# Performance work log

Measured on AMD Instinct MI355X. Metric: run time of the kernel, lower is better.

The kernel has to match this reference:

```python
import jax, jax.numpy as jnp
import numpy as np

B, T, D = 1, 1024, 2048
F_DIM = 1408
E = 8
TOPK = 2


def setup_inputs() -> dict:
    key = jax.random.key(0)
    ks = jax.random.split(key, 5)
    x = jax.random.normal(ks[0], (B, T, D), dtype=jnp.float32)
    # torch nn.Linear weight layout: [out_features, in_features]
    gate_w = jax.random.normal(ks[1], (E, D), dtype=jnp.float32) * 0.02
    gate_proj = jax.random.normal(ks[2], (E, F_DIM, D), dtype=jnp.float32) * 0.02
    up_proj = jax.random.normal(ks[3], (E, F_DIM, D), dtype=jnp.float32) * 0.02
    down_proj = jax.random.normal(ks[4], (E, D, F_DIM), dtype=jnp.float32) * 0.02
    return {"x": x, "gate_w": gate_w, "gate_proj": gate_proj,
            "up_proj": up_proj, "down_proj": down_proj}


def reference(x, gate_w, gate_proj, up_proj, down_proj):
    b, t, d = x.shape
    x_flat = x.reshape(-1, d)                                  # [N, D]
    n = x_flat.shape[0]
    # Router: top-k logits then softmax over the selected k.
    router_logits = x_flat @ gate_w.T                          # [N, E]
    top_w, sel = jax.lax.top_k(router_logits, TOPK)            # [N, K]
    top_w = jax.nn.softmax(top_w, axis=-1)                     # [N, K]
    # Scatter routing weights into dense per-token expert weights [N, E].
    tok_ids = jnp.arange(n)[:, None]
    tw = jnp.zeros((n, E), dtype=x.dtype).at[tok_ids, sel].add(top_w)
    # Dense expert compute (mathematically identical: unselected experts get
    # zero combine weight). SwiGLU per expert.
    g = jnp.einsum('nd,efd->enf', x_flat, gate_proj)           # [E, N, F]
    u = jnp.einsum('nd,efd->enf', x_flat, up_proj)             # [E, N, F]
    h = jax.nn.silu(g) * u                                     # [E, N, F]
    eo = jnp.einsum('enf,edf->end', h, down_proj)              # [E, N, D]
    out = jnp.einsum('end,ne->nd', eo, tw)                     # [N, D]
    return out.reshape(b, t, d)
```

## Files before the change

### kernel.cpp

```cpp
#include <hip/hip_runtime.h>
#include <hip/hip_bf16.h>
#include <stdint.h>

typedef __attribute__((ext_vector_type(8))) short short8;
typedef __attribute__((ext_vector_type(4))) float f32x4;
typedef unsigned int u32;
typedef unsigned short u16;

static constexpr int N_TOK = 1024;
static constexpr int DDIM = 2048;
static constexpr int FDIM = 1408;
static constexpr int NEXP = 8;
static constexpr int MAXROWS = 3072;
static constexpr int NT128 = 24;

static constexpr size_t O_META   = 0;
static constexpr size_t O_TE128  = 256;
static constexpr size_t O_TR128  = 384;
static constexpr size_t O_ROWTOK = 768;
static constexpr size_t O_TOKROWS= O_ROWTOK + (size_t)MAXROWS * 4;
static constexpr size_t O_SEL    = O_TOKROWS + 2048 * 4;
static constexpr size_t O_W      = O_SEL + 2048 * 4;
static constexpr size_t O_H      = (O_W + 2048 * 4 + 255) & ~(size_t)255;
static constexpr size_t O_EO     = O_H + (size_t)MAXROWS * FDIM * 2;

static __device__ __forceinline__ u16 f2bf(float f) {
    return __builtin_bit_cast(u16, __float2bfloat16(f));
}
static __device__ __forceinline__ float bf2f(u16 s) {
    u32 u = ((u32)s) << 16;
    return __builtin_bit_cast(float, u);
}
static __device__ __forceinline__ u32 pack2(float a, float b) {
    return (u32)f2bf(a) | ((u32)f2bf(b) << 16);
}

__global__ __launch_bounds__(256) void router_kernel(
    const float* __restrict__ x, const float* __restrict__ gw,
    int* __restrict__ sel, float* __restrict__ wout)
{
    __shared__ float xs[DDIM];
    __shared__ float lg[NEXP];
    const int tok = blockIdx.x;
    const float* xr = x + (size_t)tok * DDIM;
    for (int i = threadIdx.x; i < DDIM / 4; i += 256)
        ((float4*)xs)[i] = ((const float4*)xr)[i];
    __syncthreads();
    const int wid = threadIdx.x >> 6, lane = threadIdx.x & 63;
    for (int i = 0; i < 2; i++) {
        const int e = wid * 2 + i;
        const float* g = gw + (size_t)e * DDIM;
        float s = 0.f;
        for (int k = lane; k < DDIM; k += 64) s += xs[k] * g[k];
        for (int off = 32; off > 0; off >>= 1) s += __shfl_down(s, off);
        if (lane == 0) lg[e] = s;
    }
    __syncthreads();
    if (threadIdx.x == 0) {
        int i1 = 0;
        for (int e = 1; e < NEXP; e++) if (lg[e] > lg[i1]) i1 = e;
        int i2 = -1;
        for (int e = 0; e < NEXP; e++) {
            if (e == i1) continue;
            if (i2 < 0 || lg[e] > lg[i2]) i2 = e;
        }
        const float e2 = __expf(lg[i2] - lg[i1]);
        const float w1 = 1.f / (1.f + e2);
        sel[tok * 2] = i1; sel[tok * 2 + 1] = i2;
        wout[tok * 2] = w1; wout[tok * 2 + 1] = e2 * w1;
    }
}

__global__ __launch_bounds__(512) void build_kernel(
    const int* __restrict__ sel,
    int* __restrict__ meta, int* __restrict__ te128, int* __restrict__ tr128,
    int* __restrict__ row_tok, int* __restrict__ tok_rows)
{
    __shared__ int s0[N_TOK], s1[N_TOK];
    __shared__ u16 p0[N_TOK], p1[N_TOK];
    __shared__ int counts[NEXP], offs[NEXP];
    for (int i = threadIdx.x; i < N_TOK; i += 512) {
        s0[i] = sel[i * 2]; s1[i] = sel[i * 2 + 1];
    }
    __syncthreads();
    const int e = threadIdx.x >> 6, lane = threadIdx.x & 63;
    int base = 0;
    for (int c = 0; c < N_TOK / 64; c++) {
        const int tk = c * 64 + lane;
        const int slot = (s0[tk] == e) ? 0 : ((s1[tk] == e) ? 1 : -1);
        const unsigned long long m = __ballot(slot >= 0);
        const int pre = __popcll(m & ((1ull << lane) - 1ull));
        if (slot == 0) p0[tk] = (u16)(base + pre);
        else if (slot == 1) p1[tk] = (u16)(base + pre);
        base += __popcll(m);
    }
    if (lane == 0) counts[e] = base;
    __syncthreads();
    if (threadIdx.x == 0) {
        int off = 0, n128 = 0;
        for (int qq = 0; qq < NEXP; qq++) {
            offs[qq] = off;
            const int pc = (counts[qq] + 127) & ~127;
            for (int i = 0; i < pc / 128; i++) { te128[n128] = qq; tr128[n128] = off + i * 128; n128++; }
            off += pc;
        }
        meta[0] = n128; meta[1] = off;
    }
    __syncthreads();
    const int off = offs[e];
    for (int c = 0; c < N_TOK / 64; c++) {
        const int tk = c * 64 + lane;
        const int slot = (s0[tk] == e) ? 0 : ((s1[tk] == e) ? 1 : -1);
        if (slot >= 0) {
            const int row = off + (slot ? p1[tk] : p0[tk]);
            row_tok[row] = tk;
            tok_rows[tk * 2 + slot] = row;
        }
    }
    const int cnt = counts[e];
    const int pc = (cnt + 127) & ~127;
    for (int p = cnt + lane; p < pc; p += 64) row_tok[off + p] = -1;
}

__global__ __launch_bounds__(512, 4) void mlp1_kernel(
    const float* __restrict__ x,
    const float* __restrict__ gp, const float* __restrict__ upw,
    u16* __restrict__ h,
    const int* __restrict__ meta, const int* __restrict__ te128,
    const int* __restrict__ tr128, const int* __restrict__ row_tok)
{
    const int tile = blockIdx.y;
    const int nb = blockIdx.x;
    if (tile >= meta[0]) return;
    const int n0 = nb * 64;
    const int e = te128[tile];
    const int r0g = tr128[tile];

    __shared__ __align__(16) u16 As[2][128 * 64];
    __shared__ __align__(16) u16 Bs0[2][64 * 64];
    __shared__ __align__(16) u16 Bs1[2][64 * 64];

    const int t = threadIdx.x;
    const int r16 = t >> 4, c4 = t & 15;

    const float* arow[4]; bool avalid[4];
    #pragma unroll
    for (int i = 0; i < 4; i++) {
        const int tok = row_tok[r0g + r16 + 32 * i];
        avalid[i] = (tok >= 0);
        arow[i] = x + (size_t)(tok < 0 ? 0 : tok) * DDIM + c4 * 4;
    }
    const float* brow0[2];
    const float* brow1[2];
    {
        const float* B0 = gp + (size_t)e * FDIM * DDIM;
        const float* B1 = upw + (size_t)e * FDIM * DDIM;
        #pragma unroll
        for (int i = 0; i < 2; i++) {
            brow0[i] = B0 + (size_t)(n0 + r16 + 32 * i) * DDIM + c4 * 4;
            brow1[i] = B1 + (size_t)(n0 + r16 + 32 * i) * DDIM + c4 * 4;
        }
    }
    int sOffA[4], sOffB[2];
    #pragma unroll
    for (int i = 0; i < 4; i++) {
        const int row = r16 + 32 * i;
        sOffA[i] = row * 64 + (((c4 >> 1) ^ (row & 7)) * 8) + (c4 & 1) * 4;
    }
    #pragma unroll
    for (int i = 0; i < 2; i++) {
        const int row = r16 + 32 * i;
        sOffB[i] = row * 64 + (((c4 >> 1) ^ (row & 7)) * 8) + (c4 & 1) * 4;
    }

    const int wid = t >> 6, lane = t & 63;
    const int wm = (wid >> 1) * 32, wn = (wid & 1) * 32;
    const int lr = lane & 15, lhi = lane >> 4;

    f32x4 acc0[2][2], acc1[2][2];
    #pragma unroll
    for (int m = 0; m < 2; m++)
        #pragma unroll
        for (int n = 0; n < 2; n++) {
            acc0[m][n] = f32x4{0.f, 0.f, 0.f, 0.f};
            acc1[m][n] = f32x4{0.f, 0.f, 0.f, 0.f};
        }

    float4 pa[4], pb0[2], pb1[2];

    auto LOAD = [&](int k0) {
        #pragma unroll
        for (int i = 0; i < 4; i++)
            pa[i] = avalid[i] ? *(const float4*)(arow[i] + k0)
                              : make_float4(0.f, 0.f, 0.f, 0.f);
        #pragma unroll
        for (int i = 0; i < 2; i++) pb0[i] = *(const float4*)(brow0[i] + k0);
        #pragma unroll
        for (int i = 0; i < 2; i++) pb1[i] = *(const float4*)(brow1[i] + k0);
    };
    auto STORE = [&](int bsel) {
        #pragma unroll
        for (int i = 0; i < 4; i++) {
            uint2 v; v.x = pack2(pa[i].x, pa[i].y); v.y = pack2(pa[i].z, pa[i].w);
            *(uint2*)(&As[bsel][sOffA[i]]) = v;
        }
        #pragma unroll
        for (int i = 0; i < 2; i++) {
            uint2 v; v.x = pack2(pb0[i].x, pb0[i].y); v.y = pack2(pb0[i].z, pb0[i].w);
            *(uint2*)(&Bs0[bsel][sOffB[i]]) = v;
        }
        #pragma unroll
        for (int i = 0; i < 2; i++) {
            uint2 v; v.x = pack2(pb1[i].x, pb1[i].y); v.y = pack2(pb1[i].z, pb1[i].w);
            *(uint2*)(&Bs1[bsel][sOffB[i]]) = v;
        }
    };
    auto COMPUTE = [&](int bsel) {
        #pragma unroll
        for (int ks = 0; ks < 2; ks++) {
            short8 a[2], b0[2], b1[2];
            #pragma unroll
            for (int m = 0; m < 2; m++) {
                const int row = wm + m * 16 + lr;
                const int gr = (ks * 4 + lhi) ^ (row & 7);
                a[m] = *(const short8*)(&As[bsel][row * 64 + gr * 8]);
            }
            #pragma unroll
            for (int n = 0; n < 2; n++) {
                const int row = wn + n * 16 + lr;
                const int gr = (ks * 4 + lhi) ^ (row & 7);
                b0[n] = *(const short8*)(&Bs0[bsel][row * 64 + gr * 8]);
                b1[n] = *(const short8*)(&Bs1[bsel][row * 64 + gr * 8]);
            }
            #pragma unroll
            for (int m = 0; m < 2; m++)
                #pragma unroll
                for (int n = 0; n < 2; n++) {
                    acc0[m][n] = __builtin_amdgcn_mfma_f32_16x16x32_bf16(a[m], b0[n], acc0[m][n], 0, 0, 0);
                    acc1[m][n] = __builtin_amdgcn_mfma_f32_16x16x32_bf16(a[m], b1[n], acc1[m][n], 0, 0, 0);
                }
        }
    };

    constexpr int NT = DDIM / 64;
    LOAD(0); STORE(0);
    __syncthreads();
    for (int kt = 0; kt < NT; kt++) {
        const int cur = kt & 1;
        if (kt + 1 < NT) LOAD((kt + 1) * 64);
        COMPUTE(cur);
        if (kt + 1 < NT) {
            STORE(cur ^ 1);
            __syncthreads();
        }
    }

    #pragma unroll
    for (int m = 0; m < 2; m++) {
        const int rowb = r0g + wm + m * 16 + lhi * 4;
        #pragma unroll
        for (int n = 0; n < 2; n++) {
            const int col = n0 + wn + n * 16 + lr;
            #pragma unroll
            for (int j = 0; j < 4; j++) {
                const float g = acc0[m][n][j], u = acc1[m][n][j];
                const float hv = g / (1.f + __expf(-g)) * u;
                h[(size_t)(rowb + j) * FDIM + col] = f2bf(hv);
            }
        }
    }
}

__global__ __launch_bounds__(512, 4) void down_kernel(
    const u16* __restrict__ h, const float* __restrict__ dp,
    u16* __restrict__ eo,
    const int* __restrict__ meta, const int* __restrict__ te128,
    const int* __restrict__ tr128)
{
    const int tile = blockIdx.y;
    const int nb = blockIdx.x;
    if (tile >= meta[0]) return;
    const int n0 = nb * 128;
    const int e = te128[tile];
    const int r0g = tr128[tile];

    __shared__ __align__(16) u16 As[2][128 * 64];
    __shared__ __align__(16) u16 Bs[2][128 * 64];

    const int t = threadIdx.x;
    const int r8 = t >> 3, g8 = t & 7;
    const int r16 = t >> 4, c4 = t & 15;

    const u16* arow[2];
    int sOffA[2];
    #pragma unroll
    for (int i = 0; i < 2; i++) {
        const int row = r8 + 64 * i;
        arow[i] = h + (size_t)(r0g + row) * FDIM + g8 * 8;
        sOffA[i] = row * 64 + ((g8 ^ (row & 7)) * 8);
    }
    const float* brow[4];
    int sOffB[4];
    {
        const float* B = dp + (size_t)e * DDIM * FDIM;
        #pragma unroll
        for (int i = 0; i < 4; i++) {
            const int row = r16 + 32 * i;
            brow[i] = B + (size_t)(n0 + row) * FDIM + c4 * 4;
            sOffB[i] = row * 64 + (((c4 >> 1) ^ (row & 7)) * 8) + (c4 & 1) * 4;
        }
    }

    const int wid = t >> 6, lane = t & 63;
    const int wm = (wid >> 2) * 64, wn = (wid & 3) * 32;
    const int lr = lane & 15, lhi = lane >> 4;

    f32x4 acc[4][2];
    #pragma unroll
    for (int m = 0; m < 4; m++)
        #pragma unroll
        for (int n = 0; n < 2; n++)
            acc[m][n] = f32x4{0.f, 0.f, 0.f, 0.f};

    uint4 pa[2]; float4 pb[4];

    auto LOAD = [&](int k0) {
        #pragma unroll
        for (int i = 0; i < 2; i++) pa[i] = *(const uint4*)(arow[i] + k0);
        #pragma unroll
        for (int i = 0; i < 4; i++) pb[i] = *(const float4*)(brow[i] + k0);
    };
    auto STORE = [&](int bsel) {
        #pragma unroll
        for (int i = 0; i < 2; i++) *(uint4*)(&As[bsel][sOffA[i]]) = pa[i];
        #pragma unroll
        for (int i = 0; i < 4; i++) {
            uint2 v; v.x = pack2(pb[i].x, pb[i].y); v.y = pack2(pb[i].z, pb[i].w);
            *(uint2*)(&Bs[bsel][sOffB[i]]) = v;
        }
    };
    auto COMPUTE = [&](int bsel) {
        #pragma unroll
        for (int ks = 0; ks < 2; ks++) {
            short8 a[4], b[2];
            #pragma unroll
            for (int m = 0; m < 4; m++) {
                const int row = wm + m * 16 + lr;
                const int gr = (ks * 4 + lhi) ^ (row & 7);
                a[m] = *(const short8*)(&As[bsel][row * 64 + gr * 8]);
            }
            #pragma unroll
            for (int n = 0; n < 2; n++) {
                const int row = wn + n * 16 + lr;
                const int gr = (ks * 4 + lhi) ^ (row & 7);
                b[n] = *(const short8*)(&Bs[bsel][row * 64 + gr * 8]);
            }
            #pragma unroll
            for (int m = 0; m < 4; m++)
                #pragma unroll
                for (int n = 0; n < 2; n++)
                    acc[m][n] = __builtin_amdgcn_mfma_f32_16x16x32_bf16(a[m], b[n], acc[m][n], 0, 0, 0);
        }
    };

    constexpr int NT = FDIM / 64;
    LOAD(0); STORE(0);
    __syncthreads();
    for (int kt = 0; kt < NT; kt++) {
        const int cur = kt & 1;
        if (kt + 1 < NT) LOAD((kt + 1) * 64);
        COMPUTE(cur);
        if (kt + 1 < NT) {
            STORE(cur ^ 1);
            __syncthreads();
        }
    }

    #pragma unroll
    for (int m = 0; m < 4; m++) {
        const int rowb = r0g + wm + m * 16 + lhi * 4;
        #pragma unroll
        for (int n = 0; n < 2; n++) {
            const int col = n0 + wn + n * 16 + lr;
            #pragma unroll
            for (int j = 0; j < 4; j++)
                eo[(size_t)(rowb + j) * DDIM + col] = f2bf(acc[m][n][j]);
        }
    }
}

__global__ __launch_bounds__(256) void combine_kernel(
    const u16* __restrict__ eo, const int* __restrict__ tok_rows,
    const float* __restrict__ w, float* __restrict__ out)
{
    const int tok = blockIdx.x;
    const int r1 = tok_rows[tok * 2], r2 = tok_rows[tok * 2 + 1];
    const float w1 = w[tok * 2], w2 = w[tok * 2 + 1];
    const int d = threadIdx.x * 8;
    const uint4 a = *(const uint4*)(eo + (size_t)r1 * DDIM + d);
    const uint4 b = *(const uint4*)(eo + (size_t)r2 * DDIM + d);
    const u32 av[4] = {a.x, a.y, a.z, a.w};
    const u32 bv[4] = {b.x, b.y, b.z, b.w};
    float4 o0, o1;
    float* op[8] = {&o0.x, &o0.y, &o0.z, &o0.w, &o1.x, &o1.y, &o1.z, &o1.w};
    #pragma unroll
    for (int i = 0; i < 4; i++) {
        *op[2 * i]     = w1 * bf2f((u16)(av[i] & 0xffff)) + w2 * bf2f((u16)(bv[i] & 0xffff));
        *op[2 * i + 1] = w1 * bf2f((u16)(av[i] >> 16))    + w2 * bf2f((u16)(bv[i] >> 16));
    }
    float4* po = (float4*)(out + (size_t)tok * DDIM + d);
    po[0] = o0; po[1] = o1;
}

extern "C" void kernel_launch(void* const* d_in, const int* in_sizes, int n_in,
                              void* d_out, int out_size, void* d_ws, size_t ws_size,
                              hipStream_t stream) {
    const float* x  = (const float*)d_in[0];
    const float* gw = (const float*)d_in[1];
    const float* gp = (const float*)d_in[2];
    const float* up = (const float*)d_in[3];
    const float* dp = (const float*)d_in[4];
    float* out = (float*)d_out;
    char* ws = (char*)d_ws;

    int*   meta     = (int*)(ws + O_META);
    int*   te128    = (int*)(ws + O_TE128);
    int*   tr128    = (int*)(ws + O_TR128);
    int*   row_tok  = (int*)(ws + O_ROWTOK);
    int*   tok_rows = (int*)(ws + O_TOKROWS);
    int*   sel      = (int*)(ws + O_SEL);
    float* w        = (float*)(ws + O_W);
    u16*   h        = (u16*)(ws + O_H);
    u16*   eo       = (u16*)(ws + O_EO);

    router_kernel<<<N_TOK, 256, 0, stream>>>(x, gw, sel, w);
    build_kernel<<<1, 512, 0, stream>>>(sel, meta, te128, tr128, row_tok, tok_rows);
    mlp1_kernel<<<dim3(FDIM / 64, NT128), 512, 0, stream>>>(
        x, gp, up, h, meta, te128, tr128, row_tok);
    down_kernel<<<dim3(DDIM / 128, NT128), 512, 0, stream>>>(
        h, dp, eo, meta, te128, tr128);
    combine_kernel<<<N_TOK, 256, 0, stream>>>(eo, tok_rows, w, out);
}
```

Baseline: 196.8 us.

## Stage fp32 weights via direct global-to-LDS loads and shrink GEMM tiles

Both expert GEMM kernels now copy fp32 weight tiles straight into shared memory with global_load_lds, and convert them to bf16 when reading fragments instead of before the shared-memory store. Output tiles drop from 64/128 columns to 32 with a K step of 32, so far more blocks launch and each wave handles a single 16-row slice. The aim is to cut register staging and VALU conversion work on the load path and to raise parallelism. In exchange, each block reuses its activation tile less, activations are re-read more often, the K loop has twice as many iterations and barriers, and the per-fragment conversion is repeated.

```diff
diff --git a/kernel.cpp b/kernel.cpp
--- a/kernel.cpp
+++ b/kernel.cpp
@@ -33,6 +33,11 @@
 }
 static __device__ __forceinline__ u32 pack2(float a, float b) {
     return (u32)f2bf(a) | ((u32)f2bf(b) << 16);
+}
+static __device__ __forceinline__ void gload16(const void* g, void* l) {
+    __builtin_amdgcn_global_load_lds(
+        (const __attribute__((address_space(1))) void*)g,
+        (__attribute__((address_space(3))) void*)l, 16, 0, 0);
 }
 
 __global__ __launch_bounds__(256) void router_kernel(
@@ -122,7 +127,7 @@
     for (int p = cnt + lane; p < pc; p += 64) row_tok[off + p] = -1;
 }
 
-__global__ __launch_bounds__(512, 4) void mlp1_kernel(
+__global__ __launch_bounds__(512) void mlp1_kernel(
     const float* __restrict__ x,
     const float* __restrict__ gp, const float* __restrict__ upw,
     u16* __restrict__ h,
@@ -132,146 +137,98 @@
     const int tile = blockIdx.y;
     const int nb = blockIdx.x;
     if (tile >= meta[0]) return;
-    const int n0 = nb * 64;
+    const int n0 = nb * 32;
     const int e = te128[tile];
     const int r0g = tr128[tile];
 
-    __shared__ __align__(16) u16 As[2][128 * 64];
-    __shared__ __align__(16) u16 Bs0[2][64 * 64];
-    __shared__ __align__(16) u16 Bs1[2][64 * 64];
+    __shared__ __align__(16) u16 As[2][128 * 40];
+    __shared__ __align__(16) float Bs[2][2][32 * 32];
 
     const int t = threadIdx.x;
-    const int r16 = t >> 4, c4 = t & 15;
-
-    const float* arow[4]; bool avalid[4];
-    #pragma unroll
-    for (int i = 0; i < 4; i++) {
-        const int tok = row_tok[r0g + r16 + 32 * i];
-        avalid[i] = (tok >= 0);
-        arow[i] = x + (size_t)(tok < 0 ? 0 : tok) * DDIM + c4 * 4;
-    }
-    const float* brow0[2];
-    const float* brow1[2];
-    {
-        const float* B0 = gp + (size_t)e * FDIM * DDIM;
-        const float* B1 = upw + (size_t)e * FDIM * DDIM;
-        #pragma unroll
-        for (int i = 0; i < 2; i++) {
-            brow0[i] = B0 + (size_t)(n0 + r16 + 32 * i) * DDIM + c4 * 4;
-            brow1[i] = B1 + (size_t)(n0 + r16 + 32 * i) * DDIM + c4 * 4;
-        }
-    }
-    int sOffA[4], sOffB[2];
-    #pragma unroll
-    for (int i = 0; i < 4; i++) {
-        const int row = r16 + 32 * i;
-        sOffA[i] = row * 64 + (((c4 >> 1) ^ (row & 7)) * 8) + (c4 & 1) * 4;
-    }
-    #pragma unroll
-    for (int i = 0; i < 2; i++) {
-        const int row = r16 + 32 * i;
-        sOffB[i] = row * 64 + (((c4 >> 1) ^ (row & 7)) * 8) + (c4 & 1) * 4;
-    }
-
     const int wid = t >> 6, lane = t & 63;
-    const int wm = (wid >> 1) * 32, wn = (wid & 1) * 32;
     const int lr = lane & 15, lhi = lane >> 4;
 
-    f32x4 acc0[2][2], acc1[2][2];
-    #pragma unroll
-    for (int m = 0; m < 2; m++)
+    const int ar = t >> 2, ag = t & 3;
+    const int tokA = row_tok[r0g + ar];
+    const bool av = (tokA >= 0);
+    const float* asrc = x + (size_t)(av ? tokA : 0) * DDIM + ag * 8;
+    const int aoff = ar * 40 + ag * 8;
+
+    const int bmat = wid >> 2, wloc = wid & 3;
+    const int brow = wloc * 8 + (lane >> 3);
+    const int bgs = (lane & 7) ^ (brow & 7);
+    const float* bsrc = (bmat ? upw : gp) + (size_t)e * FDIM * DDIM
+                      + (size_t)(n0 + brow) * DDIM + bgs * 4;
+
+    f32x4 acc0[2], acc1[2];
+    acc0[0] = acc0[1] = acc1[0] = acc1[1] = f32x4{0.f, 0.f, 0.f, 0.f};
+    float4 pa0, pa1;
+
+    auto LOADA = [&](int k0) {
+        pa0 = av ? *(const float4*)(asrc + k0)     : make_float4(0.f, 0.f, 0.f, 0.f);
+        pa1 = av ? *(const float4*)(asrc + k0 + 4) : make_float4(0.f, 0.f, 0.f, 0.f);
+    };
+    auto STOREA = [&](int bsel) {
+        uint4 v;
+        v.x = pack2(pa0.x, pa0.y); v.y = pack2(pa0.z, pa0.w);
+        v.z = pack2(pa1.x, pa1.y); v.w = pack2(pa1.z, pa1.w);
+        *(uint4*)(&As[bsel][aoff]) = v;
+    };
+    auto STAGEB = [&](int bsel, int k0) {
+        gload16(bsrc + k0, &Bs[bmat][bsel][wloc * 256]);
+    };
+    auto COMPUTE = [&](int bsel) {
+        const int rowa = wid * 16 + lr;
+        const short8 a = *(const short8*)(&As[bsel][rowa * 40 + lhi * 8]);
         #pragma unroll
         for (int n = 0; n < 2; n++) {
-            acc0[m][n] = f32x4{0.f, 0.f, 0.f, 0.f};
-            acc1[m][n] = f32x4{0.f, 0.f, 0.f, 0.f};
-        }
-
-    float4 pa[4], pb0[2], pb1[2];
-
-    auto LOAD = [&](int k0) {
-        #pragma unroll
-        for (int i = 0; i < 4; i++)
-            pa[i] = avalid[i] ? *(const float4*)(arow[i] + k0)
-                              : make_float4(0.f, 0.f, 0.f, 0.f);
-        #pragma unroll
-        for (int i = 0; i < 2; i++) pb0[i] = *(const float4*)(brow0[i] + k0);
-        #pragma unroll
-        for (int i = 0; i < 2; i++) pb1[i] = *(const float4*)(brow1[i] + k0);
-    };
-    auto STORE = [&](int bsel) {
-        #pragma unroll
-        for (int i = 0; i < 4; i++) {
-            uint2 v; v.x = pack2(pa[i].x, pa[i].y); v.y = pack2(pa[i].z, pa[i].w);
-            *(uint2*)(&As[bsel][sOffA[i]]) = v;
-        }
-        #pragma unroll
-        for (int i = 0; i < 2; i++) {
-            uint2 v; v.x = pack2(pb0[i].x, pb0[i].y); v.y = pack2(pb0[i].z, pb0[i].w);
-            *(uint2*)(&Bs0[bsel][sOffB[i]]) = v;
-        }
-        #pragma unroll
-        for (int i = 0; i < 2; i++) {
-            uint2 v; v.x = pack2(pb1[i].x, pb1[i].y); v.y = pack2(pb1[i].z, pb1[i].w);
-            *(uint2*)(&Bs1[bsel][sOffB[i]]) = v;
-        }
-    };
-    auto COMPUTE = [&](int bsel) {
-        #pragma unroll
-        for (int ks = 0; ks < 2; ks++) {
-            short8 a[2], b0[2], b1[2];
+            const int rb = n * 16 + lr;
+            const int g0 = ((lhi << 1)    ) ^ (rb & 7);
+            const int g1 = ((lhi << 1) | 1) ^ (rb & 7);
             #pragma unroll
-            for (int m = 0; m < 2; m++) {
-                const int row = wm + m * 16 + lr;
-                const int gr = (ks * 4 + lhi) ^ (row & 7);
-                a[m] = *(const short8*)(&As[bsel][row * 64 + gr * 8]);
+            for (int mat = 0; mat < 2; mat++) {
+                const f32x4 lo = *(const f32x4*)(&Bs[mat][bsel][rb * 32 + g0 * 4]);
+                const f32x4 hi = *(const f32x4*)(&Bs[mat][bsel][rb * 32 + g1 * 4]);
+                uint4 q;
+                q.x = pack2(lo[0], lo[1]); q.y = pack2(lo[2], lo[3]);
+                q.z = pack2(hi[0], hi[1]); q.w = pack2(hi[2], hi[3]);
+                const short8 b = __builtin_bit_cast(short8, q);
+                if (mat == 0)
+                    acc0[n] = __builtin_amdgcn_mfma_f32_16x16x32_bf16(a, b, acc0[n], 0, 0, 0);
+                else
+                    acc1[n] = __builtin_amdgcn_mfma_f32_16x16x32_bf16(a, b, acc1[n], 0, 0, 0);
             }
-            #pragma unroll
-            for (int n = 0; n < 2; n++) {
-                const int row = wn + n * 16 + lr;
-                const int gr = (ks * 4 + lhi) ^ (row & 7);
-                b0[n] = *(const short8*)(&Bs0[bsel][row * 64 + gr * 8]);
-                b1[n] = *(const short8*)(&Bs1[bsel][row * 64 + gr * 8]);
-            }
-            #pragma unroll
-            for (int m = 0; m < 2; m++)
-                #pragma unroll
-                for (int n = 0; n < 2; n++) {
-                    acc0[m][n] = __builtin_amdgcn_mfma_f32_16x16x32_bf16(a[m], b0[n], acc0[m][n], 0, 0, 0);
-                    acc1[m][n] = __builtin_amdgcn_mfma_f32_16x16x32_bf16(a[m], b1[n], acc1[m][n], 0, 0, 0);
-                }
-        }
-    };
-
-    constexpr int NT = DDIM / 64;
-    LOAD(0); STORE(0);
+        }
+    };
+
+    constexpr int NT = DDIM / 32;
+    STAGEB(0, 0); LOADA(0); STOREA(0);
     __syncthreads();
     for (int kt = 0; kt < NT; kt++) {
         const int cur = kt & 1;
-        if (kt + 1 < NT) LOAD((kt + 1) * 64);
+        const bool more = (kt + 1 < NT);
+        if (more) { LOADA((kt + 1) * 32); STAGEB(cur ^ 1, (kt + 1) * 32); }
         COMPUTE(cur);
-        if (kt + 1 < NT) {
-            STORE(cur ^ 1);
+        if (more) {
+            STOREA(cur ^ 1);
             __syncthreads();
         }
     }
 
     #pragma unroll
-    for (int m = 0; m < 2; m++) {
-        const int rowb = r0g + wm + m * 16 + lhi * 4;
+    for (int n = 0; n < 2; n++) {
+        const int col = n0 + n * 16 + lr;
         #pragma unroll
-        for (int n = 0; n < 2; n++) {
-            const int col = n0 + wn + n * 16 + lr;
-            #pragma unroll
-            for (int j = 0; j < 4; j++) {
-                const float g = acc0[m][n][j], u = acc1[m][n][j];
-                const float hv = g / (1.f + __expf(-g)) * u;
-                h[(size_t)(rowb + j) * FDIM + col] = f2bf(hv);
-            }
-        }
-    }
-}
-
-__global__ __launch_bounds__(512, 4) void down_kernel(
+        for (int j = 0; j < 4; j++) {
+            const int row = r0g + wid * 16 + lhi * 4 + j;
+            const float g = acc0[n][j], u = acc1[n][j];
+            const float hv = g / (1.f + __expf(-g)) * u;
+            h[(size_t)row * FDIM + col] = f2bf(hv);
+        }
+    }
+}
+
+__global__ __launch_bounds__(512) void down_kernel(
     const u16* __restrict__ h, const float* __restrict__ dp,
     u16* __restrict__ eo,
     const int* __restrict__ meta, const int* __restrict__ te128,
@@ -280,111 +237,74 @@
     const int tile = blockIdx.y;
     const int nb = blockIdx.x;
     if (tile >= meta[0]) return;
-    const int n0 = nb * 128;
+    const int n0 = nb * 32;
     const int e = te128[tile];
     const int r0g = tr128[tile];
 
-    __shared__ __align__(16) u16 As[2][128 * 64];
-    __shared__ __align__(16) u16 Bs[2][128 * 64];
+    __shared__ __align__(16) u16 As[2][128 * 40];
+    __shared__ __align__(16) float Bs[2][32 * 32];
 
     const int t = threadIdx.x;
-    const int r8 = t >> 3, g8 = t & 7;
-    const int r16 = t >> 4, c4 = t & 15;
-
-    const u16* arow[2];
-    int sOffA[2];
-    #pragma unroll
-    for (int i = 0; i < 2; i++) {
-        const int row = r8 + 64 * i;
-        arow[i] = h + (size_t)(r0g + row) * FDIM + g8 * 8;
-        sOffA[i] = row * 64 + ((g8 ^ (row & 7)) * 8);
-    }
-    const float* brow[4];
-    int sOffB[4];
-    {
-        const float* B = dp + (size_t)e * DDIM * FDIM;
+    const int wid = t >> 6, lane = t & 63;
+    const int lr = lane & 15, lhi = lane >> 4;
+
+    const int ar = t >> 2, ag = t & 3;
+    const u16* asrc = h + (size_t)(r0g + ar) * FDIM + ag * 8;
+    const int aoff = ar * 40 + ag * 8;
+
+    const int brow = (wid & 3) * 8 + (lane >> 3);
+    const int bgs = (lane & 7) ^ (brow & 7);
+    const float* bsrc = dp + (size_t)e * DDIM * FDIM
+                      + (size_t)(n0 + brow) * FDIM + bgs * 4;
+
+    f32x4 acc[2];
+    acc[0] = acc[1] = f32x4{0.f, 0.f, 0.f, 0.f};
+    uint4 pa;
+
+    auto LOADA = [&](int k0u) { pa = *(const uint4*)(asrc + k0u); };
+    auto STOREA = [&](int bsel) { *(uint4*)(&As[bsel][aoff]) = pa; };
+    auto STAGEB = [&](int bsel, int k0) {
+        if (wid < 4) gload16(bsrc + k0, &Bs[bsel][(wid & 3) * 256]);
+    };
+    auto COMPUTE = [&](int bsel) {
+        const int rowa = wid * 16 + lr;
+        const short8 a = *(const short8*)(&As[bsel][rowa * 40 + lhi * 8]);
         #pragma unroll
-        for (int i = 0; i < 4; i++) {
-            const int row = r16 + 32 * i;
-            brow[i] = B + (size_t)(n0 + row) * FDIM + c4 * 4;
-            sOffB[i] = row * 64 + (((c4 >> 1) ^ (row & 7)) * 8) + (c4 & 1) * 4;
-        }
-    }
-
-    const int wid = t >> 6, lane = t & 63;
-    const int wm = (wid >> 2) * 64, wn = (wid & 3) * 32;
-    const int lr = lane & 15, lhi = lane >> 4;
-
-    f32x4 acc[4][2];
-    #pragma unroll
-    for (int m = 0; m < 4; m++)
-        #pragma unroll
-        for (int n = 0; n < 2; n++)
-            acc[m][n] = f32x4{0.f, 0.f, 0.f, 0.f};
-
-    uint4 pa[2]; float4 pb[4];
-
-    auto LOAD = [&](int k0) {
-        #pragma unroll
-        for (int i = 0; i < 2; i++) pa[i] = *(const uint4*)(arow[i] + k0);
-        #pragma unroll
-        for (int i = 0; i < 4; i++) pb[i] = *(const float4*)(brow[i] + k0);
-    };
-    auto STORE = [&](int bsel) {
-        #pragma unroll
-        for (int i = 0; i < 2; i++) *(uint4*)(&As[bsel][sOffA[i]]) = pa[i];
-        #pragma unroll
-        for (int i = 0; i < 4; i++) {
-            uint2 v; v.x = pack2(pb[i].x, pb[i].y); v.y = pack2(pb[i].z, pb[i].w);
-            *(uint2*)(&Bs[bsel][sOffB[i]]) = v;
-        }
-    };
-    auto COMPUTE = [&](int bsel) {
-        #pragma unroll
-        for (int ks = 0; ks < 2; ks++) {
-            short8 a[4], b[2];
-            #pragma unroll
-            for (int m = 0; m < 4; m++) {
-                const int row = wm + m * 16 + lr;
-                const int gr = (ks * 4 + lhi) ^ (row & 7);
-                a[m] = *(const short8*)(&As[bsel][row * 64 + gr * 8]);
-            }
-            #pragma unroll
-            for (int n = 0; n < 2; n++) {
-                const int row = wn + n * 16 + lr;
-                const int gr = (ks * 4 + lhi) ^ (row & 7);
-                b[n] = *(const short8*)(&Bs[bsel][row * 64 + gr * 8]);
-            }
-            #pragma unroll
-            for (int m = 0; m < 4; m++)
-                #pragma unroll
-                for (int n = 0; n < 2; n++)
-                    acc[m][n] = __builtin_amdgcn_mfma_f32_16x16x32_bf16(a[m], b[n], acc[m][n], 0, 0, 0);
-        }
-    };
-
-    constexpr int NT = FDIM / 64;
-    LOAD(0); STORE(0);
+        for (int n = 0; n < 2; n++) {
+            const int rb = n * 16 + lr;
+            const int g0 = ((lhi << 1)    ) ^ (rb & 7);
+            const int g1 = ((lhi << 1) | 1) ^ (rb & 7);
+            const f32x4 lo = *(const f32x4*)(&Bs[bsel][rb * 32 + g0 * 4]);
+            const f32x4 hi = *(const f32x4*)(&Bs[bsel][rb * 32 + g1 * 4]);
+            uint4 q;
+            q.x = pack2(lo[0], lo[1]); q.y = pack2(lo[2], lo[3]);
+            q.z = pack2(hi[0], hi[1]); q.w = pack2(hi[2], hi[3]);
+            const short8 b = __builtin_bit_cast(short8, q);
+            acc[n] = __builtin_amdgcn_mfma_f32_16x16x32_bf16(a, b, acc[n], 0, 0, 0);
+        }
+    };
+
+    constexpr int NT = FDIM / 32;
+    STAGEB(0, 0); LOADA(0); STOREA(0);
     __syncthreads();
     for (int kt = 0; kt < NT; kt++) {
         const int cur = kt & 1;
-        if (kt + 1 < NT) LOAD((kt + 1) * 64);
+        const bool more = (kt + 1 < NT);
+        if (more) { LOADA((kt + 1) * 32); STAGEB(cur ^ 1, (kt + 1) * 32); }
         COMPUTE(cur);
-        if (kt + 1 < NT) {
-            STORE(cur ^ 1);
+        if (more) {
+            STOREA(cur ^ 1);
             __syncthreads();
         }
     }
 
     #pragma unroll
-    for (int m = 0; m < 4; m++) {
-        const int rowb = r0g + wm + m * 16 + lhi * 4;
+    for (int n = 0; n < 2; n++) {
+        const int col = n0 + n * 16 + lr;
         #pragma unroll
-        for (int n = 0; n < 2; n++) {
-            const int col = n0 + wn + n * 16 + lr;
-            #pragma unroll
-            for (int j = 0; j < 4; j++)
-                eo[(size_t)(rowb + j) * DDIM + col] = f2bf(acc[m][n][j]);
+        for (int j = 0; j < 4; j++) {
+            const int row = r0g + wid * 16 + lhi * 4 + j;
+            eo[(size_t)row * DDIM + col] = f2bf(acc[n][j]);
         }
     }
 }
@@ -435,9 +355,9 @@
 
     router_kernel<<<N_TOK, 256, 0, stream>>>(x, gw, sel, w);
     build_kernel<<<1, 512, 0, stream>>>(sel, meta, te128, tr128, row_tok, tok_rows);
-    mlp1_kernel<<<dim3(FDIM / 64, NT128), 512, 0, stream>>>(
+    mlp1_kernel<<<dim3(FDIM / 32, NT128), 512, 0, stream>>>(
         x, gp, up, h, meta, te128, tr128, row_tok);
-    down_kernel<<<dim3(DDIM / 128, NT128), 512, 0, stream>>>(
+    down_kernel<<<dim3(DDIM / 32, NT128), 512, 0, stream>>>(
         h, dp, eo, meta, te128, tr128);
     combine_kernel<<<N_TOK, 256, 0, stream>>>(eo, tok_rows, w, out);
 }
```

Result: slower. 270.9 us (+37.7%).
